# Performance work log

Measured on AMD Instinct MI355X. Metric: run time of the kernel, lower is better.

The kernel has to match this reference:

```python
import jax, jax.numpy as jnp
import numpy as np

N_NODES = 100000
N_EDGES = 1600000
NFEAT, NHID, NCLASS = 128, 64, 40
NLAYERS = 4
P = 2.0


def setup_inputs() -> dict:
    key = jax.random.key(0)
    ks = jax.random.split(key, 10)
    x = jax.random.normal(ks[0], (N_NODES, NFEAT), dtype=jnp.float32)
    edge_index = jax.random.randint(ks[1], (2, N_EDGES), 0, N_NODES, dtype=jnp.int32)
    s_in = 1.0 / np.sqrt(NFEAT)
    s_h = 1.0 / np.sqrt(NHID)
    return {
        "x": x,
        "edge_index": edge_index,
        "enc_W": jax.random.normal(ks[2], (NHID, NFEAT), dtype=jnp.float32) * s_in,
        "enc_b": jnp.zeros((NHID,), dtype=jnp.float32),
        "conv_W": jax.random.normal(ks[3], (NHID, NHID), dtype=jnp.float32) * s_h,
        "conv_b": jnp.zeros((NHID,), dtype=jnp.float32),
        "W_skip": jax.random.normal(ks[4], (NHID, NHID), dtype=jnp.float32) * s_h,
        "dec_W": jax.random.normal(ks[5], (NCLASS, NHID), dtype=jnp.float32) * s_h,
        "dec_b": jnp.zeros((NCLASS,), dtype=jnp.float32),
    }


def _gcn_conv(X, W, b, src, dst, n):
    # PyG GCNConv: add self-loops, symmetric normalization, then X @ W^T + b
    H = X @ W.T  # [n, nhid]
    ones = jnp.ones_like(dst, dtype=X.dtype)
    deg = jax.ops.segment_sum(ones, dst, num_segments=n)  # in-degree incl. self loops
    dinv = jnp.where(deg > 0, jax.lax.rsqrt(deg), 0.0)
    norm = dinv[src] * dinv[dst]  # [E+n]
    out = jax.ops.segment_sum(norm[:, None] * H[src], dst, num_segments=n)
    return out + b


def _gamma(X, row, col, n, p):
    # G2 gating: scatter-mean over edges of sum |X[row]-X[col]|^p, then tanh.
    # (conv_gg output in the original G2 is dead code and omitted.)
    diff = jnp.sum(jnp.abs(X[row] - X[col]) ** p, axis=-1)  # [E]
    s = jax.ops.segment_sum(diff, row, num_segments=n)
    cnt = jax.ops.segment_sum(jnp.ones_like(diff), row, num_segments=n)
    return jnp.tanh(s / jnp.maximum(cnt, 1.0))  # [n]


def reference(x, edge_index, enc_W, enc_b, conv_W, conv_b, W_skip, dec_W, dec_b):
    n = x.shape[0]
    row, col = edge_index[0], edge_index[1]
    # self-loop augmented edges for GCNConv
    loop = jnp.arange(n, dtype=edge_index.dtype)
    src_sl = jnp.concatenate([row, loop])
    dst_sl = jnp.concatenate([col, loop])

    X = jax.nn.relu(x @ enc_W.T + enc_b)  # [n, nhid]
    X_init = X
    skip_val = X_init @ W_skip.T  # constant across layers

    for _ in range(NLAYERS):
        X_agg = jax.nn.relu(_gcn_conv(X, conv_W, conv_b, src_sl, dst_sl, n))
        g = _gamma(X, row, col, n, P)[:, None]  # gamma_smooth == gamma_squash (dead convs)
        denom = 1.0 + g + g
        A = 1.0 / denom
        B = g / denom
        C = g / denom
        X = A * X + B * X_agg + C * skip_val

    return X @ dec_W.T + dec_b  # [n, nclass]
```

## Files before the change

kernel.cpp:

```cpp
#include <hip/hip_runtime.h>
#include <hip/hip_bf16.h>

#define NFEAT 128
#define NHID  64
#define NCLASS 40
#define NLAYERS 4


__global__ void count_in_k(const int* __restrict__ ei, int E, int* __restrict__ cnt_col) {
    int t = blockIdx.x * blockDim.x + threadIdx.x;
    int base = t * 4;
    if (base >= E) return;
    if (base + 4 <= E) {
        int4 c4 = *reinterpret_cast<const int4*>(ei + E + base);
        atomicAdd(&cnt_col[c4.x], 1);
        atomicAdd(&cnt_col[c4.y], 1);
        atomicAdd(&cnt_col[c4.z], 1);
        atomicAdd(&cnt_col[c4.w], 1);
    } else {
        for (int e = base; e < E; ++e) atomicAdd(&cnt_col[ei[E + e]], 1);
    }
}

__global__ void dinv_k(const int* __restrict__ cnt_col, float* __restrict__ dinv, int n) {
    int v = blockIdx.x * blockDim.x + threadIdx.x;
    if (v >= n) return;
    dinv[v] = 1.0f / sqrtf((float)(cnt_col[v] + 1));
}

__global__ void scanA_k(const int* __restrict__ cnt, int* __restrict__ off,
                        int* __restrict__ bsum, int n) {
    __shared__ int t[1024];
    int i = blockIdx.x * 1024 + threadIdx.x;
    int x = (i < n) ? cnt[i] : 0;
    t[threadIdx.x] = x;
    __syncthreads();
    for (int d = 1; d < 1024; d <<= 1) {
        int y = (threadIdx.x >= (unsigned)d) ? t[threadIdx.x - d] : 0;
        __syncthreads();
        t[threadIdx.x] += y;
        __syncthreads();
    }
    if (i < n) off[i] = t[threadIdx.x] - x;
    if (threadIdx.x == 1023) bsum[blockIdx.x] = t[1023];
}

__global__ void scanB_k(int* __restrict__ bsum, int nb) {
    __shared__ int t[1024];
    int x = (threadIdx.x < (unsigned)nb) ? bsum[threadIdx.x] : 0;
    t[threadIdx.x] = x;
    __syncthreads();
    for (int d = 1; d < 1024; d <<= 1) {
        int y = (threadIdx.x >= (unsigned)d) ? t[threadIdx.x - d] : 0;
        __syncthreads();
        t[threadIdx.x] += y;
        __syncthreads();
    }
    if (threadIdx.x < (unsigned)nb) bsum[threadIdx.x] = t[threadIdx.x] - x;
}

__global__ void scanC_k(int* __restrict__ off, const int* __restrict__ bsum,
                        int* __restrict__ cur, int n, int total) {
    int i = blockIdx.x * 1024 + threadIdx.x;
    if (i < n) {
        int o = off[i] + bsum[blockIdx.x];
        off[i] = o;
        cur[i] = o;
    }
    if (i == 0) off[n] = total;
}

__global__ void fill_k(const int* __restrict__ ei, int E,
                       int* __restrict__ cur, int* __restrict__ cnt_row,
                       int* __restrict__ csr) {
    int t = blockIdx.x * blockDim.x + threadIdx.x;
    int base = t * 8;
    if (base >= E) return;
    if (base + 8 <= E) {
        int4 rA = *reinterpret_cast<const int4*>(ei + base);
        int4 rB = *reinterpret_cast<const int4*>(ei + base + 4);
        int4 cA = *reinterpret_cast<const int4*>(ei + E + base);
        int4 cB = *reinterpret_cast<const int4*>(ei + E + base + 4);
        int p0 = atomicAdd(&cur[cA.x], 1);
        int p1 = atomicAdd(&cur[cA.y], 1);
        int p2 = atomicAdd(&cur[cA.z], 1);
        int p3 = atomicAdd(&cur[cA.w], 1);
        int p4 = atomicAdd(&cur[cB.x], 1);
        int p5 = atomicAdd(&cur[cB.y], 1);
        int p6 = atomicAdd(&cur[cB.z], 1);
        int p7 = atomicAdd(&cur[cB.w], 1);
        atomicAdd(&cnt_row[rA.x], 1);
        atomicAdd(&cnt_row[rA.y], 1);
        atomicAdd(&cnt_row[rA.z], 1);
        atomicAdd(&cnt_row[rA.w], 1);
        atomicAdd(&cnt_row[rB.x], 1);
        atomicAdd(&cnt_row[rB.y], 1);
        atomicAdd(&cnt_row[rB.z], 1);
        atomicAdd(&cnt_row[rB.w], 1);
        csr[p0] = rA.x;
        csr[p1] = rA.y;
        csr[p2] = rA.z;
        csr[p3] = rA.w;
        csr[p4] = rB.x;
        csr[p5] = rB.y;
        csr[p6] = rB.z;
        csr[p7] = rB.w;
    } else {
        for (int e = base; e < E; ++e) {
            int r = ei[e];
            int p = atomicAdd(&cur[ei[E + e]], 1);
            atomicAdd(&cnt_row[r], 1);
            csr[p] = r;
        }
    }
}


template<int K, int M, bool RELU, bool BIAS>
__global__ void dense_small_k(const float* __restrict__ A, const float* __restrict__ W,
                              const float* __restrict__ b, float* __restrict__ out, int n) {
    int v = blockIdx.x * blockDim.x + threadIdx.x;
    if (v >= n) return;
    float a[K];
    const float4* ap = reinterpret_cast<const float4*>(A + (size_t)v * K);
#pragma unroll
    for (int k = 0; k < K / 4; ++k) {
        float4 t = ap[k];
        a[4 * k + 0] = t.x; a[4 * k + 1] = t.y; a[4 * k + 2] = t.z; a[4 * k + 3] = t.w;
    }
    float4* op = reinterpret_cast<float4*>(out + (size_t)v * M);
#pragma unroll 1
    for (int m = 0; m < M; m += 4) {
        float acc0 = BIAS ? b[m + 0] : 0.f;
        float acc1 = BIAS ? b[m + 1] : 0.f;
        float acc2 = BIAS ? b[m + 2] : 0.f;
        float acc3 = BIAS ? b[m + 3] : 0.f;
#pragma unroll
        for (int k = 0; k < K; ++k) {
            float av = a[k];
            acc0 = fmaf(av, W[(m + 0) * K + k], acc0);
            acc1 = fmaf(av, W[(m + 1) * K + k], acc1);
            acc2 = fmaf(av, W[(m + 2) * K + k], acc2);
            acc3 = fmaf(av, W[(m + 3) * K + k], acc3);
        }
        if (RELU) {
            acc0 = fmaxf(acc0, 0.f); acc1 = fmaxf(acc1, 0.f);
            acc2 = fmaxf(acc2, 0.f); acc3 = fmaxf(acc3, 0.f);
        }
        float4 o; o.x = acc0; o.y = acc1; o.z = acc2; o.w = acc3;
        op[m >> 2] = o;
    }
}


template<int K, int M, int MC>
__global__ void dense_enc_k(const float* __restrict__ A, const float* __restrict__ W,
                            const float* __restrict__ b, float* __restrict__ out, int n) {
    int v = blockIdx.x * blockDim.x + threadIdx.x;
    if (v >= n) return;
    const float4* ap = reinterpret_cast<const float4*>(A + (size_t)v * K);
    float4* op = reinterpret_cast<float4*>(out + (size_t)v * M);
#pragma unroll 1
    for (int mc = 0; mc < M; mc += MC) {
        float acc[MC];
#pragma unroll
        for (int m = 0; m < MC; ++m) acc[m] = b[mc + m];
#pragma unroll 1
        for (int kb = 0; kb < K / 4; ++kb) {
            float4 a4 = ap[kb];
#pragma unroll
            for (int m = 0; m < MC; ++m) {
                const float* wr = W + (size_t)(mc + m) * K + kb * 4;
                acc[m] = fmaf(a4.x, wr[0], acc[m]);
                acc[m] = fmaf(a4.y, wr[1], acc[m]);
                acc[m] = fmaf(a4.z, wr[2], acc[m]);
                acc[m] = fmaf(a4.w, wr[3], acc[m]);
            }
        }
#pragma unroll
        for (int m = 0; m < MC; m += 4) {
            float4 o;
            o.x = fmaxf(acc[m + 0], 0.f);
            o.y = fmaxf(acc[m + 1], 0.f);
            o.z = fmaxf(acc[m + 2], 0.f);
            o.w = fmaxf(acc[m + 3], 0.f);
            op[(mc + m) >> 2] = o;
        }
    }
}

__global__ void gather_k(const float* __restrict__ X, const int* __restrict__ csr,
                         const int* __restrict__ col_off, const float* __restrict__ dinv,
                         float* __restrict__ pre, float* __restrict__ gs, int n) {
    int v = blockIdx.x * 4 + (threadIdx.x >> 6);
    if (v >= n) return;
    int lane = threadIdx.x & 63;
    int grp = lane >> 4;
    int sub = lane & 15;

    float4 xv = reinterpret_cast<const float4*>(X + (size_t)v * NHID)[sub];
    int beg = col_off[v], end = col_off[v + 1];

    float4 acc = make_float4(0.f, 0.f, 0.f, 0.f);
    for (int e = beg + grp; e < end; e += 4) {
        int s = csr[e];
        float w = dinv[s];
        float4 xs = reinterpret_cast<const float4*>(X + (size_t)s * NHID)[sub];
        acc.x = fmaf(w, xs.x, acc.x);
        acc.y = fmaf(w, xs.y, acc.y);
        acc.z = fmaf(w, xs.z, acc.z);
        acc.w = fmaf(w, xs.w, acc.w);
        float dx = xs.x - xv.x;
        float part = dx * dx;
        dx = xs.y - xv.y; part = fmaf(dx, dx, part);
        dx = xs.z - xv.z; part = fmaf(dx, dx, part);
        dx = xs.w - xv.w; part = fmaf(dx, dx, part);
#pragma unroll
        for (int m = 1; m <= 8; m <<= 1) part += __shfl_xor(part, m, 64);
        if (sub == 0) atomicAdd(&gs[s], part);
    }
#pragma unroll
    for (int m = 16; m <= 32; m <<= 1) {
        acc.x += __shfl_xor(acc.x, m, 64);
        acc.y += __shfl_xor(acc.y, m, 64);
        acc.z += __shfl_xor(acc.z, m, 64);
        acc.w += __shfl_xor(acc.w, m, 64);
    }
    if (grp == 0) {
        float dv = dinv[v];
        float dv2 = dv * dv;
        float4 o;
        o.x = fmaf(dv, acc.x, dv2 * xv.x);
        o.y = fmaf(dv, acc.y, dv2 * xv.y);
        o.z = fmaf(dv, acc.z, dv2 * xv.z);
        o.w = fmaf(dv, acc.w, dv2 * xv.w);
        reinterpret_cast<float4*>(pre + (size_t)v * NHID)[sub] = o;
    }
}

__global__ void update_k(float* __restrict__ X, const float* __restrict__ pre,
                         const float* __restrict__ skip, const float* __restrict__ W,
                         const float* __restrict__ b, float* __restrict__ gs,
                         const int* __restrict__ cnt_row, int n) {
    int v = blockIdx.x * blockDim.x + threadIdx.x;
    if (v >= n) return;
    float a[NHID];
    const float4* ap = reinterpret_cast<const float4*>(pre + (size_t)v * NHID);
#pragma unroll
    for (int k = 0; k < NHID / 4; ++k) {
        float4 t = ap[k];
        a[4 * k + 0] = t.x; a[4 * k + 1] = t.y; a[4 * k + 2] = t.z; a[4 * k + 3] = t.w;
    }
    float gv = tanhf(gs[v] / fmaxf((float)cnt_row[v], 1.f));
    gs[v] = 0.f;
    float inv = 1.0f / (1.0f + 2.0f * gv);

    float4* Xp = reinterpret_cast<float4*>(X + (size_t)v * NHID);
    const float4* Sp = reinterpret_cast<const float4*>(skip + (size_t)v * NHID);
#pragma unroll 1
    for (int m = 0; m < NHID; m += 4) {
        float t0 = b[m + 0], t1 = b[m + 1], t2 = b[m + 2], t3 = b[m + 3];
#pragma unroll
        for (int k = 0; k < NHID; ++k) {
            float av = a[k];
            t0 = fmaf(av, W[(m + 0) * NHID + k], t0);
            t1 = fmaf(av, W[(m + 1) * NHID + k], t1);
            t2 = fmaf(av, W[(m + 2) * NHID + k], t2);
            t3 = fmaf(av, W[(m + 3) * NHID + k], t3);
        }
        t0 = fmaxf(t0, 0.f); t1 = fmaxf(t1, 0.f);
        t2 = fmaxf(t2, 0.f); t3 = fmaxf(t3, 0.f);
        float4 x4 = Xp[m >> 2];
        float4 s4 = Sp[m >> 2];
        float4 o;
        o.x = (x4.x + gv * (t0 + s4.x)) * inv;
        o.y = (x4.y + gv * (t1 + s4.y)) * inv;
        o.z = (x4.z + gv * (t2 + s4.z)) * inv;
        o.w = (x4.w + gv * (t3 + s4.w)) * inv;
        Xp[m >> 2] = o;
    }
}


extern "C" void kernel_launch(void* const* d_in, const int* in_sizes, int n_in,
                              void* d_out, int out_size, void* d_ws, size_t ws_size,
                              hipStream_t stream) {
    const float* x      = (const float*)d_in[0];
    const int*   ei     = (const int*)  d_in[1];
    const float* enc_W  = (const float*)d_in[2];
    const float* enc_b  = (const float*)d_in[3];
    const float* conv_W = (const float*)d_in[4];
    const float* conv_b = (const float*)d_in[5];
    const float* W_skip = (const float*)d_in[6];
    const float* dec_W  = (const float*)d_in[7];
    const float* dec_b  = (const float*)d_in[8];

    const int n = in_sizes[0] / NFEAT;
    const int E = in_sizes[1] / 2;

    char* ws = (char*)d_ws;
    auto alloc = [&](size_t bytes) {
        char* p = ws;
        ws += (bytes + 255) & ~(size_t)255;
        return p;
    };

    float* X    = (float*)alloc((size_t)n * NHID * 4);
    float* pre  = (float*)alloc((size_t)n * NHID * 4);
    float* skip = (float*)alloc((size_t)n * NHID * 4);
    float* gs   = (float*)alloc((size_t)n * 4);
    float* dinv = (float*)alloc((size_t)n * 4);
    int* cnt_row = (int*)alloc((size_t)n * 4);
    int* cnt_col = (int*)alloc((size_t)n * 4);
    int* col_off = (int*)alloc((size_t)(n + 1) * 4);
    int* cur     = (int*)alloc((size_t)n * 4);
    int* bsc     = (int*)alloc(1024 * 4);
    int* csr     = (int*)alloc((size_t)E * 4);

    hipMemsetAsync(cnt_row, 0, (size_t)n * 4, stream);
    hipMemsetAsync(cnt_col, 0, (size_t)n * 4, stream);
    hipMemsetAsync(gs, 0, (size_t)n * 4, stream);

    count_in_k<<<(E / 4 + 255) / 256, 256, 0, stream>>>(ei, E, cnt_col);
    dinv_k<<<(n + 255) / 256, 256, 0, stream>>>(cnt_col, dinv, n);

    int nb = (n + 1023) / 1024;
    scanA_k<<<nb, 1024, 0, stream>>>(cnt_col, col_off, bsc, n);
    scanB_k<<<1, 1024, 0, stream>>>(bsc, nb);
    scanC_k<<<nb, 1024, 0, stream>>>(col_off, bsc, cur, n, E);
    fill_k<<<(E / 8 + 255) / 256, 256, 0, stream>>>(ei, E, cur, cnt_row, csr);

    dense_enc_k<NFEAT, NHID, 32><<<(n + 255) / 256, 256, 0, stream>>>(x, enc_W, enc_b, X, n);
    dense_small_k<NHID, NHID, false, false><<<(n + 255) / 256, 256, 0, stream>>>(X, W_skip, nullptr, skip, n);

    for (int l = 0; l < NLAYERS; ++l) {
        gather_k<<<(n + 3) / 4, 256, 0, stream>>>(X, csr, col_off, dinv, pre, gs, n);
        update_k<<<(n + 255) / 256, 256, 0, stream>>>(X, pre, skip, conv_W, conv_b, gs, cnt_row, n);
    }

    dense_small_k<NHID, NCLASS, false, true><<<(n + 255) / 256, 256, 0, stream>>>(X, dec_W, dec_b, (float*)d_out, n);
}
```

Measured before the change: 1.052 ms.

## Build CSR via atomic ranks, fuse dinv into scan, unroll gather loop

The edge-count kernel now records each edge's rank within its destination bucket and also counts row degrees. The fill pass then becomes an atomic-free scatter using col_off plus rank, which removes the second round of atomics on the cursor array. dinv is computed inside the scan kernel, gs is zeroed there, and the dinv kernel and a memset are removed. The gather loop is unrolled by two edges per group to increase memory-level parallelism, at the cost of an extra E-sized rank buffer.

```diff
diff --git a/kernel.cpp b/kernel.cpp
--- a/kernel.cpp
+++ b/kernel.cpp
@@ -7,32 +7,39 @@
 #define NLAYERS 4
 
 
-__global__ void count_in_k(const int* __restrict__ ei, int E, int* __restrict__ cnt_col) {
+__global__ void count_rank_k(const int* __restrict__ ei, int E,
+                             int* __restrict__ cnt_col, int* __restrict__ cnt_row,
+                             int* __restrict__ rank) {
     int t = blockIdx.x * blockDim.x + threadIdx.x;
     int base = t * 4;
     if (base >= E) return;
     if (base + 4 <= E) {
         int4 c4 = *reinterpret_cast<const int4*>(ei + E + base);
-        atomicAdd(&cnt_col[c4.x], 1);
-        atomicAdd(&cnt_col[c4.y], 1);
-        atomicAdd(&cnt_col[c4.z], 1);
-        atomicAdd(&cnt_col[c4.w], 1);
+        int4 r4 = *reinterpret_cast<const int4*>(ei + base);
+        int4 k4;
+        k4.x = atomicAdd(&cnt_col[c4.x], 1);
+        k4.y = atomicAdd(&cnt_col[c4.y], 1);
+        k4.z = atomicAdd(&cnt_col[c4.z], 1);
+        k4.w = atomicAdd(&cnt_col[c4.w], 1);
+        atomicAdd(&cnt_row[r4.x], 1);
+        atomicAdd(&cnt_row[r4.y], 1);
+        atomicAdd(&cnt_row[r4.z], 1);
+        atomicAdd(&cnt_row[r4.w], 1);
+        *reinterpret_cast<int4*>(rank + base) = k4;
     } else {
-        for (int e = base; e < E; ++e) atomicAdd(&cnt_col[ei[E + e]], 1);
-    }
-}
-
-__global__ void dinv_k(const int* __restrict__ cnt_col, float* __restrict__ dinv, int n) {
-    int v = blockIdx.x * blockDim.x + threadIdx.x;
-    if (v >= n) return;
-    dinv[v] = 1.0f / sqrtf((float)(cnt_col[v] + 1));
+        for (int e = base; e < E; ++e) {
+            rank[e] = atomicAdd(&cnt_col[ei[E + e]], 1);
+            atomicAdd(&cnt_row[ei[e]], 1);
+        }
+    }
 }
 
 __global__ void scanA_k(const int* __restrict__ cnt, int* __restrict__ off,
-                        int* __restrict__ bsum, int n) {
+                        int* __restrict__ bsum, float* __restrict__ dinv, int n) {
     __shared__ int t[1024];
     int i = blockIdx.x * 1024 + threadIdx.x;
     int x = (i < n) ? cnt[i] : 0;
+    if (i < n) dinv[i] = 1.0f / sqrtf((float)(x + 1));
     t[threadIdx.x] = x;
     __syncthreads();
     for (int d = 1; d < 1024; d <<= 1) {
@@ -60,19 +67,18 @@
 }
 
 __global__ void scanC_k(int* __restrict__ off, const int* __restrict__ bsum,
-                        int* __restrict__ cur, int n, int total) {
+                        float* __restrict__ gs, int n, int total) {
     int i = blockIdx.x * 1024 + threadIdx.x;
     if (i < n) {
-        int o = off[i] + bsum[blockIdx.x];
-        off[i] = o;
-        cur[i] = o;
+        off[i] += bsum[blockIdx.x];
+        gs[i] = 0.f;
     }
     if (i == 0) off[n] = total;
 }
 
-__global__ void fill_k(const int* __restrict__ ei, int E,
-                       int* __restrict__ cur, int* __restrict__ cnt_row,
-                       int* __restrict__ csr) {
+__global__ void scatter_k(const int* __restrict__ ei, int E,
+                          const int* __restrict__ col_off, const int* __restrict__ rank,
+                          int* __restrict__ csr) {
     int t = blockIdx.x * blockDim.x + threadIdx.x;
     int base = t * 8;
     if (base >= E) return;
@@ -81,37 +87,19 @@
         int4 rB = *reinterpret_cast<const int4*>(ei + base + 4);
         int4 cA = *reinterpret_cast<const int4*>(ei + E + base);
         int4 cB = *reinterpret_cast<const int4*>(ei + E + base + 4);
-        int p0 = atomicAdd(&cur[cA.x], 1);
-        int p1 = atomicAdd(&cur[cA.y], 1);
-        int p2 = atomicAdd(&cur[cA.z], 1);
-        int p3 = atomicAdd(&cur[cA.w], 1);
-        int p4 = atomicAdd(&cur[cB.x], 1);
-        int p5 = atomicAdd(&cur[cB.y], 1);
-        int p6 = atomicAdd(&cur[cB.z], 1);
-        int p7 = atomicAdd(&cur[cB.w], 1);
-        atomicAdd(&cnt_row[rA.x], 1);
-        atomicAdd(&cnt_row[rA.y], 1);
-        atomicAdd(&cnt_row[rA.z], 1);
-        atomicAdd(&cnt_row[rA.w], 1);
-        atomicAdd(&cnt_row[rB.x], 1);
-        atomicAdd(&cnt_row[rB.y], 1);
-        atomicAdd(&cnt_row[rB.z], 1);
-        atomicAdd(&cnt_row[rB.w], 1);
-        csr[p0] = rA.x;
-        csr[p1] = rA.y;
-        csr[p2] = rA.z;
-        csr[p3] = rA.w;
-        csr[p4] = rB.x;
-        csr[p5] = rB.y;
-        csr[p6] = rB.z;
-        csr[p7] = rB.w;
+        int4 kA = *reinterpret_cast<const int4*>(rank + base);
+        int4 kB = *reinterpret_cast<const int4*>(rank + base + 4);
+        csr[col_off[cA.x] + kA.x] = rA.x;
+        csr[col_off[cA.y] + kA.y] = rA.y;
+        csr[col_off[cA.z] + kA.z] = rA.z;
+        csr[col_off[cA.w] + kA.w] = rA.w;
+        csr[col_off[cB.x] + kB.x] = rB.x;
+        csr[col_off[cB.y] + kB.y] = rB.y;
+        csr[col_off[cB.z] + kB.z] = rB.z;
+        csr[col_off[cB.w] + kB.w] = rB.w;
     } else {
-        for (int e = base; e < E; ++e) {
-            int r = ei[e];
-            int p = atomicAdd(&cur[ei[E + e]], 1);
-            atomicAdd(&cnt_row[r], 1);
-            csr[p] = r;
-        }
+        for (int e = base; e < E; ++e)
+            csr[col_off[ei[E + e]] + rank[e]] = ei[e];
     }
 }
 
@@ -202,16 +190,43 @@
     int beg = col_off[v], end = col_off[v + 1];
 
     float4 acc = make_float4(0.f, 0.f, 0.f, 0.f);
-    for (int e = beg + grp; e < end; e += 4) {
+    int e = beg + grp;
+    for (; e + 4 < end; e += 8) {
+        int s0 = csr[e];
+        int s1 = csr[e + 4];
+        float w0 = dinv[s0];
+        float w1 = dinv[s1];
+        float4 x0 = reinterpret_cast<const float4*>(X + (size_t)s0 * NHID)[sub];
+        float4 x1 = reinterpret_cast<const float4*>(X + (size_t)s1 * NHID)[sub];
+        acc.x = fmaf(w0, x0.x, acc.x); acc.y = fmaf(w0, x0.y, acc.y);
+        acc.z = fmaf(w0, x0.z, acc.z); acc.w = fmaf(w0, x0.w, acc.w);
+        acc.x = fmaf(w1, x1.x, acc.x); acc.y = fmaf(w1, x1.y, acc.y);
+        acc.z = fmaf(w1, x1.z, acc.z); acc.w = fmaf(w1, x1.w, acc.w);
+        float dx = x0.x - xv.x; float p0 = dx * dx;
+        dx = x0.y - xv.y; p0 = fmaf(dx, dx, p0);
+        dx = x0.z - xv.z; p0 = fmaf(dx, dx, p0);
+        dx = x0.w - xv.w; p0 = fmaf(dx, dx, p0);
+        dx = x1.x - xv.x; float p1 = dx * dx;
+        dx = x1.y - xv.y; p1 = fmaf(dx, dx, p1);
+        dx = x1.z - xv.z; p1 = fmaf(dx, dx, p1);
+        dx = x1.w - xv.w; p1 = fmaf(dx, dx, p1);
+#pragma unroll
+        for (int m = 1; m <= 8; m <<= 1) {
+            p0 += __shfl_xor(p0, m, 64);
+            p1 += __shfl_xor(p1, m, 64);
+        }
+        if (sub == 0) {
+            atomicAdd(&gs[s0], p0);
+            atomicAdd(&gs[s1], p1);
+        }
+    }
+    if (e < end) {
         int s = csr[e];
         float w = dinv[s];
         float4 xs = reinterpret_cast<const float4*>(X + (size_t)s * NHID)[sub];
-        acc.x = fmaf(w, xs.x, acc.x);
-        acc.y = fmaf(w, xs.y, acc.y);
-        acc.z = fmaf(w, xs.z, acc.z);
-        acc.w = fmaf(w, xs.w, acc.w);
-        float dx = xs.x - xv.x;
-        float part = dx * dx;
+        acc.x = fmaf(w, xs.x, acc.x); acc.y = fmaf(w, xs.y, acc.y);
+        acc.z = fmaf(w, xs.z, acc.z); acc.w = fmaf(w, xs.w, acc.w);
+        float dx = xs.x - xv.x; float part = dx * dx;
         dx = xs.y - xv.y; part = fmaf(dx, dx, part);
         dx = xs.z - xv.z; part = fmaf(dx, dx, part);
         dx = xs.w - xv.w; part = fmaf(dx, dx, part);
@@ -313,22 +328,20 @@
     int* cnt_row = (int*)alloc((size_t)n * 4);
     int* cnt_col = (int*)alloc((size_t)n * 4);
     int* col_off = (int*)alloc((size_t)(n + 1) * 4);
-    int* cur     = (int*)alloc((size_t)n * 4);
+    int* rank    = (int*)alloc((size_t)E * 4);
     int* bsc     = (int*)alloc(1024 * 4);
     int* csr     = (int*)alloc((size_t)E * 4);
 
     hipMemsetAsync(cnt_row, 0, (size_t)n * 4, stream);
     hipMemsetAsync(cnt_col, 0, (size_t)n * 4, stream);
-    hipMemsetAsync(gs, 0, (size_t)n * 4, stream);
-
-    count_in_k<<<(E / 4 + 255) / 256, 256, 0, stream>>>(ei, E, cnt_col);
-    dinv_k<<<(n + 255) / 256, 256, 0, stream>>>(cnt_col, dinv, n);
+
+    count_rank_k<<<(E / 4 + 255) / 256, 256, 0, stream>>>(ei, E, cnt_col, cnt_row, rank);
 
     int nb = (n + 1023) / 1024;
-    scanA_k<<<nb, 1024, 0, stream>>>(cnt_col, col_off, bsc, n);
+    scanA_k<<<nb, 1024, 0, stream>>>(cnt_col, col_off, bsc, dinv, n);
     scanB_k<<<1, 1024, 0, stream>>>(bsc, nb);
-    scanC_k<<<nb, 1024, 0, stream>>>(col_off, bsc, cur, n, E);
-    fill_k<<<(E / 8 + 255) / 256, 256, 0, stream>>>(ei, E, cur, cnt_row, csr);
+    scanC_k<<<nb, 1024, 0, stream>>>(col_off, bsc, gs, n, E);
+    scatter_k<<<(E / 8 + 255) / 256, 256, 0, stream>>>(ei, E, col_off, rank, csr);
 
     dense_enc_k<NFEAT, NHID, 32><<<(n + 255) / 256, 256, 0, stream>>>(x, enc_W, enc_b, X, n);
     dense_small_k<NHID, NHID, false, false><<<(n + 255) / 256, 256, 0, stream>>>(X, W_skip, nullptr, skip, n);
```

Measured after the change: 966.4 us. -8.1%, faster.
